# Kernel optimization log

Hardware: AMD Instinct MI355X
Metric: run time of the kernel (lower is better)

## Reference

```python
import jax, jax.numpy as jnp
import numpy as np

B, CIN, COUT, H, W, K, SDIM = 16, 256, 256, 64, 64, 3, 128

def setup_inputs() -> dict:
    key = jax.random.key(0)
    ks = jax.random.split(key, 5)
    return {
        "x": jax.random.normal(ks[0], (B, CIN, H, W), dtype=jnp.float32),
        "c_src": jax.random.normal(ks[1], (B, SDIM), dtype=jnp.float32),
        "c_trg": jax.random.normal(ks[2], (B, SDIM), dtype=jnp.float32),
        "style_w": jax.random.normal(ks[3], (CIN, SDIM), dtype=jnp.float32),
        "style_b": jnp.ones((CIN,), dtype=jnp.float32),  # bias_init=1
        "weight": jax.random.normal(ks[4], (1, COUT, CIN, K, K), dtype=jnp.float32),
    }

def reference(x, c_src, c_trg, style_w, style_b, weight):
    b, cin, h, w = x.shape
    _, cout, _, k, _ = weight.shape
    # EqualLinear: scale = 1/sqrt(dim_in)=1/sqrt(128), lr_mul=1
    lin_scale = np.float32(1.0 / np.sqrt(SDIM))
    s = c_trg @ (style_w * lin_scale).T + style_b            # [B, Cin]
    # modulate
    conv_scale = np.float32(1.0 / np.sqrt(cin * k * k))
    wmod = conv_scale * weight * s[:, None, :, None, None]   # [B, Cout, Cin, K, K]
    # demodulate
    demod = jax.lax.rsqrt(jnp.sum(wmod * wmod, axis=(2, 3, 4)) + 1e-8)  # [B, Cout]
    wmod = wmod * demod[:, :, None, None, None]
    # grouped conv with groups=batch == per-sample conv; vmap over batch
    def conv_one(xb, wb):
        # xb: [Cin,H,W], wb: [Cout,Cin,K,K]
        return jax.lax.conv_general_dilated(
            xb[None], wb, window_strides=(1, 1), padding="SAME",
            dimension_numbers=("NCHW", "OIHW", "NCHW"))[0]
    out = jax.vmap(conv_one)(x, wmod)                        # [B, Cout, H, W]
    return out
```

## Files before the change

### kernel.cpp

```cpp
#include <hip/hip_runtime.h>


#define WSH_OFF    35684352
#define S_OFF      36864000
#define G_OFF      36880384
#define DEMOD_OFF  37142528

typedef __attribute__((ext_vector_type(8))) short bf16x8;
typedef __attribute__((ext_vector_type(4))) float f32x4;
typedef __attribute__((ext_vector_type(4))) int i32x4;

#define GLOAD_LDS16(g, l)                                                        \
  __builtin_amdgcn_global_load_lds(                                              \
      (const __attribute__((address_space(1))) void*)(g),                        \
      (__attribute__((address_space(3))) void*)(l), 16, 0, 0)

__device__ __forceinline__ unsigned short f2bf(float f) {
  unsigned int u = __builtin_bit_cast(unsigned int, f);
  u += 0x7FFFu + ((u >> 16) & 1u);
  return (unsigned short)(u >> 16);
}

__global__ void prep1_k(const float* __restrict__ c_trg,
                        const float* __restrict__ style_w,
                        const float* __restrict__ style_b,
                        const float* __restrict__ weight,
                        float* __restrict__ s,
                        short* __restrict__ wsh,
                        float* __restrict__ G) {
  const int blk = blockIdx.x;
  const int tid = threadIdx.x;
  if (blk < 16) {
    const int b = blk;
    const float* ct = c_trg + b * 128;
    const float* sw = style_w + tid * 128;
    float acc = 0.f;
#pragma unroll 4
    for (int d = 0; d < 128; ++d) acc += ct[d] * sw[d];
    s[b * 256 + tid] = acc * 0.08838834764831845f + style_b[tid];
  } else {
    const int idx = (blk - 16) * 256 + tid;
    const float* wsrc = weight + idx * 9;
    float g = 0.f;
#pragma unroll
    for (int t = 0; t < 9; ++t) {
      float v = wsrc[t] * 0.020833333333333332f;
      g += v * v;
      wsh[t * 65536 + idx] = (short)f2bf(v);
    }
    G[idx] = g;
  }
}

__global__ void demod_k(const float* __restrict__ G,
                        const float* __restrict__ s,
                        float* __restrict__ demod) {
  const int bid = blockIdx.x;
  const int b = bid >> 8, co = bid & 255;
  const int t = threadIdx.x;
  const float sv = s[b * 256 + t];
  float ss = G[co * 256 + t] * sv * sv;
#pragma unroll
  for (int o = 32; o; o >>= 1) ss += __shfl_down(ss, o);
  __shared__ float red[4];
  if ((t & 63) == 0) red[t >> 6] = ss;
  __syncthreads();
  if (t == 0) demod[bid] = rsqrtf(red[0] + red[1] + red[2] + red[3] + 1e-8f);
}

__global__ void xpose_k(const float* __restrict__ x,
                        const float* __restrict__ s,
                        short* __restrict__ xpad) {
  __shared__ float tile[64][65];
  const int bid = blockIdx.x;
  const int tid = threadIdx.x;
  if (bid >= 4096) {
    const int b = bid - 4096;
    char* base = (char*)xpad + b * 66 * 66 * 512;
    const i32x4 z = {0, 0, 0, 0};
    for (int i = tid; i < 4224; i += 256) {
      const int r = i >= 2112;
      const int off = r * (65 * 66 * 512) + (i - r * 2112) * 16;
      *(i32x4*)(base + off) = z;
    }
    for (int i = tid; i < 4096; i += 256) {
      const int h = 1 + (i >> 6);
      const int side = (i >> 5) & 1;
      const int j = i & 31;
      *(i32x4*)(base + (h * 66 + side * 65) * 512 + j * 16) = z;
    }
    return;
  }
  const int ct = bid & 3;
  const int h = (bid >> 2) & 63;
  const int b = bid >> 8;
  const int w = tid & 63, cl = tid >> 6;
  const float* src = x + ((b * 256 + ct * 64) * 64 + h) * 64;
#pragma unroll
  for (int i = 0; i < 16; ++i) {
    int c = i * 4 + cl;
    tile[c][w] = src[c * 4096 + w];
  }
  const int cp = tid & 31;
  const float s0 = s[b * 256 + ct * 64 + cp * 2];
  const float s1 = s[b * 256 + ct * 64 + cp * 2 + 1];
  __syncthreads();
  short* dst = xpad + ((b * 66 + h + 1) * 66 + 1) * 256 + ct * 64;
#pragma unroll
  for (int i = 0; i < 8; ++i) {
    int idx = i * 256 + tid;
    int w2 = idx >> 5;
    unsigned int u = (unsigned int)f2bf(tile[cp * 2][w2] * s0) |
                     ((unsigned int)f2bf(tile[cp * 2 + 1][w2] * s1) << 16);
    *(unsigned int*)(dst + w2 * 256 + cp * 2) = u;
  }
}

__global__ __launch_bounds__(512, 2) void conv_k(const short* __restrict__ xpad,
                                                 const short* __restrict__ wsh,
                                                 const float* __restrict__ demod,
                                                 float* __restrict__ out) {
  extern __shared__ __align__(16) char lds[];

  const int tid = threadIdx.x;
  const int lane = tid & 63;
  const int wid = tid >> 6;
  const int wm = wid >> 2;
  const int wn = wid & 3;

  const int orig = blockIdx.x;
  const int bid = (orig & 7) * 32 + (orig >> 3);
  const int b = bid >> 4;
  const int r0 = (bid & 15) * 4;

  const int t3 = tid >> 3;
  const int c16 = (tid & 7) * 16;
  const int swzc = c16 ^ ((t3 & 7) << 4);
  int aBase[4], bBase[4];
#pragma unroll
  for (int i = 0; i < 4; ++i) {
    aBase[i] = (i * 64 + t3) * 512 + swzc;
    bBase[i] = ((b * 66 + r0 + i) * 66 + t3) * 512 + swzc;
  }
  const char* wB = (const char*)wsh;
  const char* xB = (const char*)xpad;

  auto stage = [&](int kk, int d) {
    const int tap = kk >> 2, cc = kk & 3;
    const int dh = (tap * 11) >> 5;
    const int dw = tap - dh * 3;
    const int aO = tap * 131072 + cc * 128;
    const int bO = (dh * 66 + dw) * 512 + cc * 128;
    char* ldsT = lds + d * 65536;
#pragma unroll
    for (int i = 0; i < 4; ++i)
      GLOAD_LDS16(wB + aO + aBase[i], ldsT + (i * 512 + tid) * 16);
#pragma unroll
    for (int i = 0; i < 4; ++i)
      GLOAD_LDS16(xB + bO + bBase[i], ldsT + 32768 + (i * 512 + tid) * 16);
  };

  const int xall = (lane & 7) << 4;
  const int xl = xall & 0x30;
  const int xh = xall & 0x40;
  const int colR = (((lane >> 4) << 4) ^ xl);
  const int ksOff0 = xh;
  const int ksOff1 = 64 ^ xh;
  const int aRd = (wm * 128 + (lane & 15)) * 128 + colR;
  const int bRd = 32768 + (wn * 64 + (lane & 15)) * 128 + colR;

  f32x4 acc[8][4] = {};

  stage(0, 0);
  stage(1, 1);

  for (int kk = 0; kk < 36; ++kk) {
    if (kk == 35) {
      asm volatile("s_waitcnt vmcnt(0)" ::: "memory");
    } else {
      asm volatile("s_waitcnt vmcnt(8)" ::: "memory");
    }
    __builtin_amdgcn_s_barrier();
    __builtin_amdgcn_sched_barrier(0);

    const char* Ab = lds + (kk & 1) * 65536 + aRd;
    const char* Bb = lds + (kk & 1) * 65536 + bRd;
#pragma unroll
    for (int ks = 0; ks < 2; ++ks) {
      const int ko = ks ? ksOff1 : ksOff0;
      bf16x8 af[8], bfr[4];
#pragma unroll
      for (int m = 0; m < 8; ++m) af[m] = *(const bf16x8*)(Ab + m * 2048 + ko);
#pragma unroll
      for (int n = 0; n < 4; ++n) bfr[n] = *(const bf16x8*)(Bb + n * 2048 + ko);
      __builtin_amdgcn_s_setprio(1);
#pragma unroll
      for (int m = 0; m < 8; ++m)
#pragma unroll
        for (int n = 0; n < 4; ++n)
          acc[m][n] = __builtin_amdgcn_mfma_f32_16x16x32_bf16(af[m], bfr[n], acc[m][n], 0, 0, 0);
      __builtin_amdgcn_s_setprio(0);
    }

    asm volatile("s_waitcnt lgkmcnt(0)" ::: "memory");
    __builtin_amdgcn_s_barrier();
    __builtin_amdgcn_sched_barrier(0);
    asm volatile("" ::: "memory");
    if (kk + 2 < 36) stage(kk + 2, kk & 1);
  }

  const int pc = lane & 15;
  const int rOff = (lane >> 4) * 4;
  const int h = r0 + wn;
#pragma unroll
  for (int m = 0; m < 8; ++m) {
#pragma unroll
    for (int r = 0; r < 4; ++r) {
      const int co = wm * 128 + m * 16 + rOff + r;
      const float dm = demod[(b << 8) + co];
      float* orow = out + (((b << 8) + co) << 12) + (h << 6);
#pragma unroll
      for (int n = 0; n < 4; ++n) {
        orow[n * 16 + pc] = acc[m][n][r] * dm;
      }
    }
  }
}

extern "C" void kernel_launch(void* const* d_in, const int* in_sizes, int n_in,
                              void* d_out, int out_size, void* d_ws, size_t ws_size,
                              hipStream_t stream) {
  const float* x       = (const float*)d_in[0];
  const float* c_trg   = (const float*)d_in[2];
  const float* style_w = (const float*)d_in[3];
  const float* style_b = (const float*)d_in[4];
  const float* weight  = (const float*)d_in[5];
  float* out = (float*)d_out;

  char* ws = (char*)d_ws;
  short* xpad  = (short*)(ws);
  short* wsh   = (short*)(ws + WSH_OFF);
  float* s     = (float*)(ws + S_OFF);
  float* G     = (float*)(ws + G_OFF);
  float* demod = (float*)(ws + DEMOD_OFF);

  hipFuncSetAttribute((const void*)conv_k,
                      hipFuncAttributeMaxDynamicSharedMemorySize, 131072);

  prep1_k<<<272, 256, 0, stream>>>(c_trg, style_w, style_b, weight, s, wsh, G);
  demod_k<<<4096, 256, 0, stream>>>(G, s, demod);
  xpose_k<<<4112, 256, 0, stream>>>(x, s, xpad);
  conv_k<<<256, 512, 131072, stream>>>(xpad, wsh, demod, out);
}
```

Measured before the change: 106.8 us.

## Deepen conv K-pipeline to 4-stage ring with interleaved split loads

The conv main loop now uses 32-channel K-slices instead of 64, held in a 4-buffer LDS ring with prefetch depth 3, so there are 72 iterations instead of 36. Each iteration needs only one barrier. The weight and activation global-to-LDS loads for a future slice are issued between the two halves of the MFMA work. The XOR swizzle on LDS rows is removed, which shortens address math but may add LDS bank conflicts on the 64-byte-stride rows.

```diff
diff --git a/kernel.cpp b/kernel.cpp
--- a/kernel.cpp
+++ b/kernel.cpp
@@ -133,80 +133,88 @@
   const int b = bid >> 4;
   const int r0 = (bid & 15) * 4;
 
-  const int t3 = tid >> 3;
-  const int c16 = (tid & 7) * 16;
-  const int swzc = c16 ^ ((t3 & 7) << 4);
-  int aBase[4], bBase[4];
-#pragma unroll
-  for (int i = 0; i < 4; ++i) {
-    aBase[i] = (i * 64 + t3) * 512 + swzc;
-    bBase[i] = ((b * 66 + r0 + i) * 66 + t3) * 512 + swzc;
-  }
+  const int t2 = tid >> 2;
+  const int c4b = (tid & 3) * 16;
+  const int aO0 = t2 * 512 + c4b;
+  const int aO1 = aO0 + 65536;
+  const int bO0 = ((b * 66 + r0 + (t2 >> 6)) * 66 + (t2 & 63)) * 512 + c4b;
+  const int bO1 = bO0 + 67584;
   const char* wB = (const char*)wsh;
   const char* xB = (const char*)xpad;
 
-  auto stage = [&](int kk, int d) {
-    const int tap = kk >> 2, cc = kk & 3;
-    const int dh = (tap * 11) >> 5;
-    const int dw = tap - dh * 3;
-    const int aO = tap * 131072 + cc * 128;
-    const int bO = (dh * 66 + dw) * 512 + cc * 128;
-    char* ldsT = lds + d * 65536;
-#pragma unroll
-    for (int i = 0; i < 4; ++i)
-      GLOAD_LDS16(wB + aO + aBase[i], ldsT + (i * 512 + tid) * 16);
-#pragma unroll
-    for (int i = 0; i < 4; ++i)
-      GLOAD_LDS16(xB + bO + bBase[i], ldsT + 32768 + (i * 512 + tid) * 16);
-  };
-
-  const int xall = (lane & 7) << 4;
-  const int xl = xall & 0x30;
-  const int xh = xall & 0x40;
-  const int colR = (((lane >> 4) << 4) ^ xl);
-  const int ksOff0 = xh;
-  const int ksOff1 = 64 ^ xh;
-  const int aRd = (wm * 128 + (lane & 15)) * 128 + colR;
-  const int bRd = 32768 + (wn * 64 + (lane & 15)) * 128 + colR;
+  const int aRdBase = (wm * 128 + (lane & 15)) * 64 + (lane >> 4) * 16;
+  const int bRdBase = 16384 + (wn * 64 + (lane & 15)) * 64 + (lane >> 4) * 16;
 
   f32x4 acc[8][4] = {};
 
-  stage(0, 0);
-  stage(1, 1);
-
-  for (int kk = 0; kk < 36; ++kk) {
-    if (kk == 35) {
-      asm volatile("s_waitcnt vmcnt(0)" ::: "memory");
-    } else {
-      asm volatile("s_waitcnt vmcnt(8)" ::: "memory");
-    }
+#pragma unroll
+  for (int t = 0; t < 3; ++t) {
+    const int cc = t;
+    const int aAdd = cc * 64;
+    const int bAdd = cc * 64;
+    char* dA = lds + t * 32768;
+    GLOAD_LDS16(wB + aAdd + aO0, dA + tid * 16);
+    GLOAD_LDS16(wB + aAdd + aO1, dA + 8192 + tid * 16);
+    GLOAD_LDS16(xB + bAdd + bO0, dA + 16384 + tid * 16);
+    GLOAD_LDS16(xB + bAdd + bO1, dA + 24576 + tid * 16);
+  }
+
+  for (int t = 0; t < 72; ++t) {
+    if (t < 70)       asm volatile("s_waitcnt vmcnt(8)" ::: "memory");
+    else if (t == 70) asm volatile("s_waitcnt vmcnt(4)" ::: "memory");
+    else              asm volatile("s_waitcnt vmcnt(0)" ::: "memory");
     __builtin_amdgcn_s_barrier();
     __builtin_amdgcn_sched_barrier(0);
 
-    const char* Ab = lds + (kk & 1) * 65536 + aRd;
-    const char* Bb = lds + (kk & 1) * 65536 + bRd;
-#pragma unroll
-    for (int ks = 0; ks < 2; ++ks) {
-      const int ko = ks ? ksOff1 : ksOff0;
-      bf16x8 af[8], bfr[4];
-#pragma unroll
-      for (int m = 0; m < 8; ++m) af[m] = *(const bf16x8*)(Ab + m * 2048 + ko);
-#pragma unroll
-      for (int n = 0; n < 4; ++n) bfr[n] = *(const bf16x8*)(Bb + n * 2048 + ko);
-      __builtin_amdgcn_s_setprio(1);
-#pragma unroll
-      for (int m = 0; m < 8; ++m)
-#pragma unroll
-        for (int n = 0; n < 4; ++n)
-          acc[m][n] = __builtin_amdgcn_mfma_f32_16x16x32_bf16(af[m], bfr[n], acc[m][n], 0, 0, 0);
-      __builtin_amdgcn_s_setprio(0);
+    const char* Ab = lds + (t & 3) * 32768 + aRdBase;
+    const char* Bb = lds + (t & 3) * 32768 + bRdBase;
+    bf16x8 af[8], bfr[4];
+#pragma unroll
+    for (int m = 0; m < 4; ++m) af[m] = *(const bf16x8*)(Ab + m * 1024);
+#pragma unroll
+    for (int n = 0; n < 4; ++n) bfr[n] = *(const bf16x8*)(Bb + n * 1024);
+
+    const int ts = t + 3;
+    if (ts < 72) {
+      const int tap = ts >> 3, cc = ts & 7;
+      const int aAdd = tap * 131072 + cc * 64;
+      char* dA = lds + (ts & 3) * 32768;
+      asm volatile("" ::: "memory");
+      GLOAD_LDS16(wB + aAdd + aO0, dA + tid * 16);
+      GLOAD_LDS16(wB + aAdd + aO1, dA + 8192 + tid * 16);
     }
 
     asm volatile("s_waitcnt lgkmcnt(0)" ::: "memory");
-    __builtin_amdgcn_s_barrier();
     __builtin_amdgcn_sched_barrier(0);
-    asm volatile("" ::: "memory");
-    if (kk + 2 < 36) stage(kk + 2, kk & 1);
+    __builtin_amdgcn_s_setprio(1);
+#pragma unroll
+    for (int m = 0; m < 4; ++m)
+#pragma unroll
+      for (int n = 0; n < 4; ++n)
+        acc[m][n] = __builtin_amdgcn_mfma_f32_16x16x32_bf16(af[m], bfr[n], acc[m][n], 0, 0, 0);
+    __builtin_amdgcn_s_setprio(0);
+
+#pragma unroll
+    for (int m = 4; m < 8; ++m) af[m] = *(const bf16x8*)(Ab + m * 1024);
+    if (ts < 72) {
+      const int tap = ts >> 3, cc = ts & 7;
+      const int dh = (tap * 11) >> 5;
+      const int bAdd = (dh * 66 + (tap - dh * 3)) * 512 + cc * 64;
+      char* dB = lds + (ts & 3) * 32768 + 16384;
+      asm volatile("" ::: "memory");
+      GLOAD_LDS16(xB + bAdd + bO0, dB + tid * 16);
+      GLOAD_LDS16(xB + bAdd + bO1, dB + 8192 + tid * 16);
+    }
+
+    asm volatile("s_waitcnt lgkmcnt(0)" ::: "memory");
+    __builtin_amdgcn_sched_barrier(0);
+    __builtin_amdgcn_s_setprio(1);
+#pragma unroll
+    for (int m = 4; m < 8; ++m)
+#pragma unroll
+      for (int n = 0; n < 4; ++n)
+        acc[m][n] = __builtin_amdgcn_mfma_f32_16x16x32_bf16(af[m], bfr[n], acc[m][n], 0, 0, 0);
+    __builtin_amdgcn_s_setprio(0);
   }
 
   const int pc = lane & 15;
```

Result: slower. 110.5 us (+3.4%).

## Interleave conv main loop into four MFMA quadrants with staged prefetch; fuse demod into xpose

Applied to the files above, without the earlier changes.

The conv loop drops the two-stage-ahead prefetch and instead loads only the next step's tiles. The A and B tile loads are issued from inside the current step, between four quadrant MFMA phases that are separated by barriers, with a full vmcnt(0) wait at the end of each step. The aim is to interleave LDS reads and global-to-LDS traffic with MFMA work and to lower register pressure by holding only half of the A and B fragments at once. The demod reduction also moves into extra blocks of the xpose kernel, removing one kernel launch. The cost is many more barriers per iteration and a shallower prefetch depth, which may expose global load latency.

```diff
diff --git a/kernel.cpp b/kernel.cpp
--- a/kernel.cpp
+++ b/kernel.cpp
@@ -52,28 +52,27 @@
   }
 }
 
-__global__ void demod_k(const float* __restrict__ G,
-                        const float* __restrict__ s,
-                        float* __restrict__ demod) {
-  const int bid = blockIdx.x;
-  const int b = bid >> 8, co = bid & 255;
-  const int t = threadIdx.x;
-  const float sv = s[b * 256 + t];
-  float ss = G[co * 256 + t] * sv * sv;
-#pragma unroll
-  for (int o = 32; o; o >>= 1) ss += __shfl_down(ss, o);
-  __shared__ float red[4];
-  if ((t & 63) == 0) red[t >> 6] = ss;
-  __syncthreads();
-  if (t == 0) demod[bid] = rsqrtf(red[0] + red[1] + red[2] + red[3] + 1e-8f);
-}
-
 __global__ void xpose_k(const float* __restrict__ x,
                         const float* __restrict__ s,
-                        short* __restrict__ xpad) {
+                        const float* __restrict__ G,
+                        short* __restrict__ xpad,
+                        float* __restrict__ demod) {
   __shared__ float tile[64][65];
   const int bid = blockIdx.x;
   const int tid = threadIdx.x;
+  if (bid >= 4112) {
+    const int id = bid - 4112;
+    const int b = id >> 8, co = id & 255;
+    const float sv = s[b * 256 + tid];
+    float ss = G[co * 256 + tid] * sv * sv;
+#pragma unroll
+    for (int o = 32; o; o >>= 1) ss += __shfl_down(ss, o);
+    __shared__ float red[4];
+    if ((tid & 63) == 0) red[tid >> 6] = ss;
+    __syncthreads();
+    if (tid == 0) demod[id] = rsqrtf(red[0] + red[1] + red[2] + red[3] + 1e-8f);
+    return;
+  }
   if (bid >= 4096) {
     const int b = bid - 4096;
     char* base = (char*)xpad + b * 66 * 66 * 512;
@@ -136,77 +135,131 @@
   const int t3 = tid >> 3;
   const int c16 = (tid & 7) * 16;
   const int swzc = c16 ^ ((t3 & 7) << 4);
-  int aBase[4], bBase[4];
-#pragma unroll
-  for (int i = 0; i < 4; ++i) {
-    aBase[i] = (i * 64 + t3) * 512 + swzc;
-    bBase[i] = ((b * 66 + r0 + i) * 66 + t3) * 512 + swzc;
+  int aO[4], bO[4];
+#pragma unroll
+  for (int j = 0; j < 4; ++j) {
+    aO[j] = (j * 64 + t3) * 512 + swzc;
+    bO[j] = ((b * 66 + r0 + j) * 66 + t3) * 512 + swzc;
   }
   const char* wB = (const char*)wsh;
   const char* xB = (const char*)xpad;
 
-  auto stage = [&](int kk, int d) {
-    const int tap = kk >> 2, cc = kk & 3;
+  auto stageA = [&](int ts) {
+    const int tap = ts >> 2, cc = ts & 3;
+    const int aAdd = tap * 131072 + cc * 128;
+    char* d = lds + (ts & 1) * 65536;
+#pragma unroll
+    for (int j = 0; j < 4; ++j)
+      GLOAD_LDS16(wB + aAdd + aO[j], d + j * 8192 + tid * 16);
+  };
+  auto stageB = [&](int ts) {
+    const int tap = ts >> 2, cc = ts & 3;
     const int dh = (tap * 11) >> 5;
-    const int dw = tap - dh * 3;
-    const int aO = tap * 131072 + cc * 128;
-    const int bO = (dh * 66 + dw) * 512 + cc * 128;
-    char* ldsT = lds + d * 65536;
-#pragma unroll
-    for (int i = 0; i < 4; ++i)
-      GLOAD_LDS16(wB + aO + aBase[i], ldsT + (i * 512 + tid) * 16);
-#pragma unroll
-    for (int i = 0; i < 4; ++i)
-      GLOAD_LDS16(xB + bO + bBase[i], ldsT + 32768 + (i * 512 + tid) * 16);
+    const int bAdd = (dh * 66 + (tap - dh * 3)) * 512 + cc * 128;
+    char* d = lds + (ts & 1) * 65536 + 32768;
+#pragma unroll
+    for (int j = 0; j < 4; ++j)
+      GLOAD_LDS16(xB + bAdd + bO[j], d + j * 8192 + tid * 16);
   };
 
   const int xall = (lane & 7) << 4;
   const int xl = xall & 0x30;
   const int xh = xall & 0x40;
   const int colR = (((lane >> 4) << 4) ^ xl);
-  const int ksOff0 = xh;
-  const int ksOff1 = 64 ^ xh;
-  const int aRd = (wm * 128 + (lane & 15)) * 128 + colR;
-  const int bRd = 32768 + (wn * 64 + (lane & 15)) * 128 + colR;
+  const int ko0 = xh;
+  const int ko1 = 64 ^ xh;
+  const int aRdBase = (wm * 128 + (lane & 15)) * 128 + colR;
+  const int bRdBase = 32768 + (wn * 64 + (lane & 15)) * 128 + colR;
 
   f32x4 acc[8][4] = {};
 
-  stage(0, 0);
-  stage(1, 1);
-
-  for (int kk = 0; kk < 36; ++kk) {
-    if (kk == 35) {
-      asm volatile("s_waitcnt vmcnt(0)" ::: "memory");
-    } else {
-      asm volatile("s_waitcnt vmcnt(8)" ::: "memory");
-    }
-    __builtin_amdgcn_s_barrier();
+  stageA(0);
+  stageB(0);
+  asm volatile("s_waitcnt vmcnt(0)" ::: "memory");
+  __builtin_amdgcn_s_barrier();
+  asm volatile("" ::: "memory");
+
+  for (int t = 0; t < 36; ++t) {
+    const char* Ab = lds + (t & 1) * 65536 + aRdBase;
+    const char* Bb = lds + (t & 1) * 65536 + bRdBase;
+    bf16x8 af[4][2], bq[2][2], bq2[2][2];
+
+#pragma unroll
+    for (int m = 0; m < 4; ++m) {
+      af[m][0] = *(const bf16x8*)(Ab + m * 2048 + ko0);
+      af[m][1] = *(const bf16x8*)(Ab + m * 2048 + ko1);
+    }
+#pragma unroll
+    for (int n = 0; n < 2; ++n) {
+      bq[n][0] = *(const bf16x8*)(Bb + n * 2048 + ko0);
+      bq[n][1] = *(const bf16x8*)(Bb + n * 2048 + ko1);
+    }
+    if (t + 1 < 36) stageA(t + 1);
+    __builtin_amdgcn_s_barrier();
+    asm volatile("s_waitcnt lgkmcnt(0)" ::: "memory");
     __builtin_amdgcn_sched_barrier(0);
-
-    const char* Ab = lds + (kk & 1) * 65536 + aRd;
-    const char* Bb = lds + (kk & 1) * 65536 + bRd;
-#pragma unroll
-    for (int ks = 0; ks < 2; ++ks) {
-      const int ko = ks ? ksOff1 : ksOff0;
-      bf16x8 af[8], bfr[4];
-#pragma unroll
-      for (int m = 0; m < 8; ++m) af[m] = *(const bf16x8*)(Ab + m * 2048 + ko);
-#pragma unroll
-      for (int n = 0; n < 4; ++n) bfr[n] = *(const bf16x8*)(Bb + n * 2048 + ko);
-      __builtin_amdgcn_s_setprio(1);
-#pragma unroll
-      for (int m = 0; m < 8; ++m)
-#pragma unroll
-        for (int n = 0; n < 4; ++n)
-          acc[m][n] = __builtin_amdgcn_mfma_f32_16x16x32_bf16(af[m], bfr[n], acc[m][n], 0, 0, 0);
-      __builtin_amdgcn_s_setprio(0);
-    }
-
+    __builtin_amdgcn_s_setprio(1);
+#pragma unroll
+    for (int m = 0; m < 4; ++m)
+#pragma unroll
+      for (int n = 0; n < 2; ++n) {
+        acc[m][n] = __builtin_amdgcn_mfma_f32_16x16x32_bf16(af[m][0], bq[n][0], acc[m][n], 0, 0, 0);
+        acc[m][n] = __builtin_amdgcn_mfma_f32_16x16x32_bf16(af[m][1], bq[n][1], acc[m][n], 0, 0, 0);
+      }
+    __builtin_amdgcn_s_setprio(0);
+    __builtin_amdgcn_s_barrier();
+
+#pragma unroll
+    for (int n = 0; n < 2; ++n) {
+      bq2[n][0] = *(const bf16x8*)(Bb + (n + 2) * 2048 + ko0);
+      bq2[n][1] = *(const bf16x8*)(Bb + (n + 2) * 2048 + ko1);
+    }
+    if (t + 1 < 36) stageB(t + 1);
+    __builtin_amdgcn_s_barrier();
     asm volatile("s_waitcnt lgkmcnt(0)" ::: "memory");
-    __builtin_amdgcn_s_barrier();
     __builtin_amdgcn_sched_barrier(0);
+    __builtin_amdgcn_s_setprio(1);
+#pragma unroll
+    for (int m = 0; m < 4; ++m)
+#pragma unroll
+      for (int n = 0; n < 2; ++n) {
+        acc[m][n + 2] = __builtin_amdgcn_mfma_f32_16x16x32_bf16(af[m][0], bq2[n][0], acc[m][n + 2], 0, 0, 0);
+        acc[m][n + 2] = __builtin_amdgcn_mfma_f32_16x16x32_bf16(af[m][1], bq2[n][1], acc[m][n + 2], 0, 0, 0);
+      }
+    __builtin_amdgcn_s_setprio(0);
+    __builtin_amdgcn_s_barrier();
+
+#pragma unroll
+    for (int m = 0; m < 4; ++m) {
+      af[m][0] = *(const bf16x8*)(Ab + (m + 4) * 2048 + ko0);
+      af[m][1] = *(const bf16x8*)(Ab + (m + 4) * 2048 + ko1);
+    }
+    __builtin_amdgcn_s_barrier();
+    asm volatile("s_waitcnt lgkmcnt(0)" ::: "memory");
+    __builtin_amdgcn_sched_barrier(0);
+    __builtin_amdgcn_s_setprio(1);
+#pragma unroll
+    for (int m = 0; m < 4; ++m)
+#pragma unroll
+      for (int n = 0; n < 2; ++n) {
+        acc[m + 4][n] = __builtin_amdgcn_mfma_f32_16x16x32_bf16(af[m][0], bq[n][0], acc[m + 4][n], 0, 0, 0);
+        acc[m + 4][n] = __builtin_amdgcn_mfma_f32_16x16x32_bf16(af[m][1], bq[n][1], acc[m + 4][n], 0, 0, 0);
+      }
+    __builtin_amdgcn_s_setprio(0);
+    __builtin_amdgcn_s_barrier();
+
+    __builtin_amdgcn_s_setprio(1);
+#pragma unroll
+    for (int m = 0; m < 4; ++m)
+#pragma unroll
+      for (int n = 0; n < 2; ++n) {
+        acc[m + 4][n + 2] = __builtin_amdgcn_mfma_f32_16x16x32_bf16(af[m][0], bq2[n][0], acc[m + 4][n + 2], 0, 0, 0);
+        acc[m + 4][n + 2] = __builtin_amdgcn_mfma_f32_16x16x32_bf16(af[m][1], bq2[n][1], acc[m + 4][n + 2], 0, 0, 0);
+      }
+    __builtin_amdgcn_s_setprio(0);
+    asm volatile("s_waitcnt vmcnt(0)" ::: "memory");
+    __builtin_amdgcn_s_barrier();
     asm volatile("" ::: "memory");
-    if (kk + 2 < 36) stage(kk + 2, kk & 1);
   }
 
   const int pc = lane & 15;
@@ -248,7 +301,6 @@
                       hipFuncAttributeMaxDynamicSharedMemorySize, 131072);
 
   prep1_k<<<272, 256, 0, stream>>>(c_trg, style_w, style_b, weight, s, wsh, G);
-  demod_k<<<4096, 256, 0, stream>>>(G, s, demod);
-  xpose_k<<<4112, 256, 0, stream>>>(x, s, xpad);
+  xpose_k<<<8208, 256, 0, stream>>>(x, s, G, xpad, demod);
   conv_k<<<256, 512, 131072, stream>>>(xpad, wsh, demod, out);
 }
```

Measured after the change: 101.8 us. -4.7%, faster.
